# Optimization experiments

Measured on AMD Instinct MI355X. Metric: run time of the kernel, lower is better.

The kernel has to match this reference:

```python
import math
import jax, jax.numpy as jnp
import numpy as np
from jax import lax

N = 224
EPS_BN = 1e-5


def _conv(x, w, b):
    y = lax.conv_general_dilated(x, w, (1, 1), 'SAME',
                                 dimension_numbers=('NCHW', 'OIHW', 'NCHW'))
    return y + b[None, :, None, None]


def _bn(x, g, beta, m, v):
    # eval-mode BatchNorm2d with running stats
    inv = lax.rsqrt(v + EPS_BN)
    return (x - m[None, :, None, None]) * (g * inv)[None, :, None, None] + beta[None, :, None, None]


def _maxpool2(x):
    return lax.reduce_window(x, -jnp.inf, lax.max, (1, 1, 2, 2), (1, 1, 2, 2), 'VALID')


def setup_inputs() -> dict:
    key = jax.random.key(0)
    ks = jax.random.split(key, 12)
    idx = np.arange(N, dtype=np.float32)
    angles = 2.0 * math.pi * idx[None, :] * idx[:, None] / N
    inp = {
        'sequences': jax.random.normal(ks[0], (16, 8, 3, N, N), dtype=jnp.float32),
        'dft_cos': jnp.asarray(np.cos(angles), dtype=jnp.float32),
        'dft_sin': jnp.asarray(np.sin(angles), dtype=jnp.float32),
        'conv1_w': jax.random.normal(ks[1], (16, 3, 3, 3), dtype=jnp.float32) * 0.1,
        'conv1_b': jnp.zeros((16,), jnp.float32),
        'bn1_g': jnp.ones((16,), jnp.float32),
        'bn1_b': jnp.zeros((16,), jnp.float32),
        'bn1_m': jnp.zeros((16,), jnp.float32),
        'bn1_v': jnp.ones((16,), jnp.float32),
        'conv2_w': jax.random.normal(ks[2], (32, 16, 3, 3), dtype=jnp.float32) * 0.05,
        'conv2_b': jnp.zeros((32,), jnp.float32),
        'bn2_g': jnp.ones((32,), jnp.float32),
        'bn2_b': jnp.zeros((32,), jnp.float32),
        'bn2_m': jnp.zeros((32,), jnp.float32),
        'bn2_v': jnp.ones((32,), jnp.float32),
        'conv3_w': jax.random.normal(ks[3], (64, 32, 3, 3), dtype=jnp.float32) * 0.05,
        'conv3_b': jnp.zeros((64,), jnp.float32),
        'bn3_g': jnp.ones((64,), jnp.float32),
        'bn3_b': jnp.zeros((64,), jnp.float32),
        'bn3_m': jnp.zeros((64,), jnp.float32),
        'bn3_v': jnp.ones((64,), jnp.float32),
        'fc_w': jax.random.normal(ks[4], (128, 64), dtype=jnp.float32) * 0.1,
        'fc_b': jnp.zeros((128,), jnp.float32),
    }
    return inp


def reference(sequences, dft_cos, dft_sin,
              conv1_w, conv1_b, bn1_g, bn1_b, bn1_m, bn1_v,
              conv2_w, conv2_b, bn2_g, bn2_b, bn2_m, bn2_v,
              conv3_w, conv3_b, bn3_g, bn3_b, bn3_m, bn3_v,
              fc_w, fc_b):
    b, s = sequences.shape[0], sequences.shape[1]
    x = sequences[:, s // 2]  # center frames [B,3,H,W]

    # 2D DFT via dense matmul chain: X = (C - jS) x (C - jS)
    C, S = dft_cos, dft_sin
    Cx = jnp.einsum('ij,bcjk->bcik', C, x)
    Sx = jnp.einsum('ij,bcjk->bcik', S, x)
    X_real = jnp.einsum('bcij,jk->bcik', Cx, C) - jnp.einsum('bcij,jk->bcik', Sx, S)
    X_imag = -(jnp.einsum('bcij,jk->bcik', Cx, S) + jnp.einsum('bcij,jk->bcik', Sx, C))
    magnitude = jnp.sqrt(X_real ** 2 + X_imag ** 2 + 1e-08)
    spec = jnp.log(magnitude + 1e-08)
    half = N // 2
    spec = jnp.roll(spec, shift=(half, half), axis=(-2, -1))  # fftshift

    # CNN stack (eval-mode BN, dropout disabled)
    h = jax.nn.relu(_bn(_conv(spec, conv1_w, conv1_b), bn1_g, bn1_b, bn1_m, bn1_v))
    h = _maxpool2(h)
    h = jax.nn.relu(_bn(_conv(h, conv2_w, conv2_b), bn2_g, bn2_b, bn2_m, bn2_v))
    h = _maxpool2(h)
    h = jax.nn.relu(_bn(_conv(h, conv3_w, conv3_b), bn3_g, bn3_b, bn3_m, bn3_v))
    h = jnp.mean(h, axis=(2, 3))  # AdaptiveAvgPool2d((1,1)) + flatten -> [B,64]

    freq_out = jax.nn.relu(h @ fc_w.T + fc_b)  # dropout = identity in eval
    return freq_out
```

## Files before the change

kernel.cpp:

```cpp
#include <hip/hip_runtime.h>
#include <math.h>
#include <stddef.h>

#define N224 224
#define PIX 50176
#define ROWS113 25312

__global__ __launch_bounds__(64) void dft1(
    const float* __restrict__ seq, const float* __restrict__ Cm,
    const float* __restrict__ Sm, float* __restrict__ Cx, float* __restrict__ Sx)
{
  const int p = blockIdx.z;
  const int b = p / 3, ch = p % 3;
  const float* __restrict__ x = seq + ((((size_t)b * 8 + 4) * 3 + ch) * PIX);
  const int i0 = blockIdx.y * 32;
  const int k0 = blockIdx.x * 32;
  const int tid = threadIdx.x;
  const int tx = tid & 7, ty = tid >> 3;
  __shared__ float Ctt[16][36], Stt[16][36], Xt[16][36];
  float aC[4][4], aS[4][4];
#pragma unroll
  for (int a = 0; a < 4; ++a)
#pragma unroll
    for (int d = 0; d < 4; ++d) { aC[a][d] = 0.f; aS[a][d] = 0.f; }

  const int sr = tid >> 1;
  const int sk = (tid & 1) * 8;
  const int xj = tid >> 2;
  const int xk = (tid & 3) * 8;

  const float* xbase = x  + (size_t)xj * N224 + k0 + xk;
  const float* cbase = Cm + (size_t)(i0 + sr) * N224 + sk;
  const float* sbase = Sm + (size_t)(i0 + sr) * N224 + sk;

  float4 rx0 = *(const float4*)(xbase);
  float4 rx1 = *(const float4*)(xbase + 4);
  float4 rc0 = *(const float4*)(cbase);
  float4 rc1 = *(const float4*)(cbase + 4);
  float4 rs0 = *(const float4*)(sbase);
  float4 rs1 = *(const float4*)(sbase + 4);

  for (int jt = 0; jt < 14; ++jt) {
    __syncthreads();
    *(float4*)&Xt[xj][xk]     = rx0;
    *(float4*)&Xt[xj][xk + 4] = rx1;
    Ctt[sk+0][sr]=rc0.x; Ctt[sk+1][sr]=rc0.y; Ctt[sk+2][sr]=rc0.z; Ctt[sk+3][sr]=rc0.w;
    Ctt[sk+4][sr]=rc1.x; Ctt[sk+5][sr]=rc1.y; Ctt[sk+6][sr]=rc1.z; Ctt[sk+7][sr]=rc1.w;
    Stt[sk+0][sr]=rs0.x; Stt[sk+1][sr]=rs0.y; Stt[sk+2][sr]=rs0.z; Stt[sk+3][sr]=rs0.w;
    Stt[sk+4][sr]=rs1.x; Stt[sk+5][sr]=rs1.y; Stt[sk+6][sr]=rs1.z; Stt[sk+7][sr]=rs1.w;
    __syncthreads();
    if (jt < 13) {
      const int j = (jt + 1) * 16;
      rx0 = *(const float4*)(xbase + (size_t)j * N224);
      rx1 = *(const float4*)(xbase + (size_t)j * N224 + 4);
      rc0 = *(const float4*)(cbase + j);
      rc1 = *(const float4*)(cbase + j + 4);
      rs0 = *(const float4*)(sbase + j);
      rs1 = *(const float4*)(sbase + j + 4);
    }
#pragma unroll
    for (int jj = 0; jj < 16; ++jj) {
      const float4 cv4 = *(const float4*)&Ctt[jj][4*ty];
      const float4 sv4 = *(const float4*)&Stt[jj][4*ty];
      const float4 xv4 = *(const float4*)&Xt[jj][4*tx];
      const float cva[4] = {cv4.x, cv4.y, cv4.z, cv4.w};
      const float sva[4] = {sv4.x, sv4.y, sv4.z, sv4.w};
      const float xva[4] = {xv4.x, xv4.y, xv4.z, xv4.w};
#pragma unroll
      for (int a = 0; a < 4; ++a)
#pragma unroll
        for (int d = 0; d < 4; ++d) {
          aC[a][d] = fmaf(cva[a], xva[d], aC[a][d]);
          aS[a][d] = fmaf(sva[a], xva[d], aS[a][d]);
        }
    }
  }
  const size_t b113 = (size_t)p * ROWS113;
#pragma unroll
  for (int a = 0; a < 4; ++a) {
    const int i = i0 + 4*ty + a;
    if (i <= 112) {
      const size_t off = b113 + (size_t)i * N224 + k0 + 4*tx;
      *(float4*)&Cx[off] = make_float4(aC[a][0], aC[a][1], aC[a][2], aC[a][3]);
      *(float4*)&Sx[off] = make_float4(aS[a][0], aS[a][1], aS[a][2], aS[a][3]);
    }
  }
}

__global__ __launch_bounds__(64) void dft2(
    const float* __restrict__ Cx, const float* __restrict__ Sx,
    const float* __restrict__ Cm, const float* __restrict__ Sm,
    float* __restrict__ spec)
{
  const int p = blockIdx.z;
  const int i0 = blockIdx.y * 32;
  const int k0 = blockIdx.x * 32;
  const int tid = threadIdx.x;
  const int tx = tid & 7, ty = tid >> 3;
  const size_t b113 = (size_t)p * ROWS113;
  __shared__ float CxT[16][36], SxT[16][36], Ct[16][36], St[16][36];
  float p1[4][4], p2[4][4], p3[4][4], p4[4][4];
#pragma unroll
  for (int a = 0; a < 4; ++a)
#pragma unroll
    for (int d = 0; d < 4; ++d) { p1[a][d]=0.f; p2[a][d]=0.f; p3[a][d]=0.f; p4[a][d]=0.f; }

  const int sr = tid >> 1;
  const int sk = (tid & 1) * 8;
  const int ri = (i0 + sr > 112) ? 112 : i0 + sr;
  const int xj = tid >> 2;
  const int xk = (tid & 3) * 8;

  const float* cxb = Cx + b113 + (size_t)ri * N224 + sk;
  const float* sxb = Sx + b113 + (size_t)ri * N224 + sk;
  const float* ccb = Cm + (size_t)xj * N224 + k0 + xk;
  const float* ssb = Sm + (size_t)xj * N224 + k0 + xk;

  float4 ra0 = *(const float4*)(cxb);
  float4 ra1 = *(const float4*)(cxb + 4);
  float4 rb0 = *(const float4*)(sxb);
  float4 rb1 = *(const float4*)(sxb + 4);
  float4 rc0 = *(const float4*)(ccb);
  float4 rc1 = *(const float4*)(ccb + 4);
  float4 rd0 = *(const float4*)(ssb);
  float4 rd1 = *(const float4*)(ssb + 4);

  for (int jt = 0; jt < 14; ++jt) {
    __syncthreads();
    *(float4*)&Ct[xj][xk]     = rc0;  *(float4*)&Ct[xj][xk + 4] = rc1;
    *(float4*)&St[xj][xk]     = rd0;  *(float4*)&St[xj][xk + 4] = rd1;
    CxT[sk+0][sr]=ra0.x; CxT[sk+1][sr]=ra0.y; CxT[sk+2][sr]=ra0.z; CxT[sk+3][sr]=ra0.w;
    CxT[sk+4][sr]=ra1.x; CxT[sk+5][sr]=ra1.y; CxT[sk+6][sr]=ra1.z; CxT[sk+7][sr]=ra1.w;
    SxT[sk+0][sr]=rb0.x; SxT[sk+1][sr]=rb0.y; SxT[sk+2][sr]=rb0.z; SxT[sk+3][sr]=rb0.w;
    SxT[sk+4][sr]=rb1.x; SxT[sk+5][sr]=rb1.y; SxT[sk+6][sr]=rb1.z; SxT[sk+7][sr]=rb1.w;
    __syncthreads();
    if (jt < 13) {
      const int j = (jt + 1) * 16;
      ra0 = *(const float4*)(cxb + j);
      ra1 = *(const float4*)(cxb + j + 4);
      rb0 = *(const float4*)(sxb + j);
      rb1 = *(const float4*)(sxb + j + 4);
      rc0 = *(const float4*)(ccb + (size_t)j * N224);
      rc1 = *(const float4*)(ccb + (size_t)j * N224 + 4);
      rd0 = *(const float4*)(ssb + (size_t)j * N224);
      rd1 = *(const float4*)(ssb + (size_t)j * N224 + 4);
    }
#pragma unroll
    for (int jj = 0; jj < 16; ++jj) {
      const float4 cx4 = *(const float4*)&CxT[jj][4*ty];
      const float4 sx4 = *(const float4*)&SxT[jj][4*ty];
      const float4 cc4 = *(const float4*)&Ct[jj][4*tx];
      const float4 ss4 = *(const float4*)&St[jj][4*tx];
      const float cxa[4] = {cx4.x, cx4.y, cx4.z, cx4.w};
      const float sxa[4] = {sx4.x, sx4.y, sx4.z, sx4.w};
      const float cca[4] = {cc4.x, cc4.y, cc4.z, cc4.w};
      const float ssa[4] = {ss4.x, ss4.y, ss4.z, ss4.w};
#pragma unroll
      for (int a = 0; a < 4; ++a)
#pragma unroll
        for (int d = 0; d < 4; ++d) {
          p1[a][d] = fmaf(cxa[a], cca[d], p1[a][d]);
          p2[a][d] = fmaf(sxa[a], ssa[d], p2[a][d]);
          p3[a][d] = fmaf(cxa[a], ssa[d], p3[a][d]);
          p4[a][d] = fmaf(sxa[a], cca[d], p4[a][d]);
        }
    }
  }
  const size_t sb = (size_t)p * PIX;
  const int kk0 = k0 + 4*tx;
  const int ok0 = (kk0 < 112) ? kk0 + 112 : kk0 - 112;
#pragma unroll
  for (int a = 0; a < 4; ++a) {
    const int i = i0 + 4*ty + a;
    if (i > 112) continue;
    float sp1[4], sp2[4];
#pragma unroll
    for (int d = 0; d < 4; ++d) {
      const float re = p1[a][d] - p2[a][d];
      const float im = p3[a][d] + p4[a][d];
      sp1[d] = logf(sqrtf(fmaf(re, re, fmaf(im, im, 1e-8f))) + 1e-8f);
      const float re2 = p1[a][d] + p2[a][d];
      const float im2 = p3[a][d] - p4[a][d];
      sp2[d] = logf(sqrtf(fmaf(re2, re2, fmaf(im2, im2, 1e-8f))) + 1e-8f);
    }
    const int oi = (i < 112) ? i + 112 : i - 112;
    *(float4*)&spec[sb + (size_t)oi * N224 + ok0] =
        make_float4(sp1[0], sp1[1], sp1[2], sp1[3]);
    if (i >= 1 && i <= 111)
      *(float4*)&spec[sb + (size_t)(112 - i) * N224 + ok0] =
          make_float4(sp2[0], sp2[1], sp2[2], sp2[3]);
  }
}

__global__ __launch_bounds__(256) void conv1_band(
    const float* __restrict__ spec, const float* __restrict__ w,
    const float* __restrict__ cb, const float* __restrict__ g,
    const float* __restrict__ be, const float* __restrict__ mm,
    const float* __restrict__ vv, float* __restrict__ out)
{
  const int band = blockIdx.x;
  const int b    = blockIdx.y;
  const int tid  = threadIdx.x;
  const int co   = tid & 15;
  const int q    = tid >> 4;
  const int cy0  = band * 2;
  __shared__ float in_t[3][4][228];
  __shared__ float wt[3][9][16];
  for (int i = tid; i < 3*4*224; i += 256) {
    const int x = i % 224, r = (i / 224) % 4, cc = i / 896;
    const int y = cy0 - 1 + r;
    float v = 0.f;
    if (y >= 0 && y < 224)
      v = spec[((size_t)b*3 + cc) * PIX + (size_t)y * N224 + x];
    in_t[cc][r][x+1] = v;
  }
  if (tid < 12) { const int cc = tid / 4, r = tid % 4;
                  in_t[cc][r][0] = 0.f; in_t[cc][r][225] = 0.f; }
  for (int i = tid; i < 3*9*16; i += 256) {
    const int coi = i & 15, k = (i >> 4) % 9, cc = i / 144;
    wt[cc][k][coi] = w[coi*27 + cc*9 + k];
  }
  __syncthreads();
  float acc[2][14];
#pragma unroll
  for (int i = 0; i < 2; ++i)
#pragma unroll
    for (int jx = 0; jx < 14; ++jx) acc[i][jx] = 0.f;
  const int x0 = q * 14;
#pragma unroll
  for (int cc = 0; cc < 3; ++cc) {
    float wr[9];
#pragma unroll
    for (int k = 0; k < 9; ++k) wr[k] = wt[cc][k][co];
#pragma unroll
    for (int rr = 0; rr < 4; ++rr) {
      float xr[16];
      const float2* rp = (const float2*)(&in_t[cc][rr][x0]);
#pragma unroll
      for (int t = 0; t < 8; ++t) { const float2 v = rp[t]; xr[2*t] = v.x; xr[2*t+1] = v.y; }
#pragma unroll
      for (int crow = 0; crow < 2; ++crow) {
        const int krow = rr - crow;
        if (krow < 0 || krow > 2) continue;
#pragma unroll
        for (int xx = 0; xx < 14; ++xx) {
          acc[crow][xx] = fmaf(xr[xx  ], wr[krow*3  ], acc[crow][xx]);
          acc[crow][xx] = fmaf(xr[xx+1], wr[krow*3+1], acc[crow][xx]);
          acc[crow][xx] = fmaf(xr[xx+2], wr[krow*3+2], acc[crow][xx]);
        }
      }
    }
  }
  const float s  = g[co] * rsqrtf(vv[co] + 1e-5f);
  const float sh = be[co] - mm[co]*s;
  const float bb = cb[co];
  const int px0 = q * 7;
#pragma unroll
  for (int px = 0; px < 7; ++px) {
    const float v0 = (acc[0][2*px  ] + bb)*s + sh;
    const float v1 = (acc[0][2*px+1] + bb)*s + sh;
    const float v2 = (acc[1][2*px  ] + bb)*s + sh;
    const float v3 = (acc[1][2*px+1] + bb)*s + sh;
    out[(((size_t)b*16 + co)*112 + band)*112 + px0+px] =
        fmaxf(fmaxf(fmaxf(v0, v1), fmaxf(v2, v3)), 0.f);
  }
}

__global__ __launch_bounds__(256) void conv2_band(
    const float* __restrict__ h1, const float* __restrict__ w,
    const float* __restrict__ cb, const float* __restrict__ g,
    const float* __restrict__ be, const float* __restrict__ mm,
    const float* __restrict__ vv, float* __restrict__ out)
{
  const int band = blockIdx.x;
  const int b    = blockIdx.y;
  const int tid  = threadIdx.x;
  const int co   = tid & 31;
  const int q    = tid >> 5;
  const int cy0  = band * 2;
  __shared__ float in_t[8][4][114];
  __shared__ float wt[8][9][32];
  float acc[2][14];
#pragma unroll
  for (int i = 0; i < 2; ++i)
#pragma unroll
    for (int jx = 0; jx < 14; ++jx) acc[i][jx] = 0.f;

  for (int chunk = 0; chunk < 2; ++chunk) {
    const int ci0 = chunk * 8;
    __syncthreads();
    for (int i = tid; i < 8*4*112; i += 256) {
      const int x = i % 112, r = (i / 112) % 4, cc = i / 448;
      const int y = cy0 - 1 + r;
      float v = 0.f;
      if (y >= 0 && y < 112)
        v = h1[(((size_t)b*16 + ci0+cc)*112 + y)*112 + x];
      in_t[cc][r][x+1] = v;
    }
    if (tid < 32) { const int cc = tid >> 2, r = tid & 3;
                    in_t[cc][r][0] = 0.f; in_t[cc][r][113] = 0.f; }
    for (int i = tid; i < 8*9*32; i += 256) {
      const int coi = i & 31, k = (i >> 5) % 9, cc = i / 288;
      wt[cc][k][coi] = w[coi*144 + (ci0+cc)*9 + k];
    }
    __syncthreads();
    const int x0 = q * 14;
    for (int cc = 0; cc < 8; ++cc) {
      float wr[9];
#pragma unroll
      for (int k = 0; k < 9; ++k) wr[k] = wt[cc][k][co];
#pragma unroll
      for (int rr = 0; rr < 4; ++rr) {
        float xr[16];
        const float2* rp = (const float2*)(&in_t[cc][rr][x0]);
#pragma unroll
        for (int t = 0; t < 8; ++t) { const float2 v = rp[t]; xr[2*t] = v.x; xr[2*t+1] = v.y; }
#pragma unroll
        for (int crow = 0; crow < 2; ++crow) {
          const int krow = rr - crow;
          if (krow < 0 || krow > 2) continue;
#pragma unroll
          for (int x = 0; x < 14; ++x) {
            acc[crow][x] = fmaf(xr[x  ], wr[krow*3  ], acc[crow][x]);
            acc[crow][x] = fmaf(xr[x+1], wr[krow*3+1], acc[crow][x]);
            acc[crow][x] = fmaf(xr[x+2], wr[krow*3+2], acc[crow][x]);
          }
        }
      }
    }
  }
  const float s  = g[co] * rsqrtf(vv[co] + 1e-5f);
  const float sh = be[co] - mm[co]*s;
  const float bb = cb[co];
  const int px0 = q * 7;
#pragma unroll
  for (int px = 0; px < 7; ++px) {
    const float v0 = (acc[0][2*px  ] + bb)*s + sh;
    const float v1 = (acc[0][2*px+1] + bb)*s + sh;
    const float v2 = (acc[1][2*px  ] + bb)*s + sh;
    const float v3 = (acc[1][2*px+1] + bb)*s + sh;
    out[(((size_t)b*32 + co)*56 + band)*56 + px0+px] =
        fmaxf(fmaxf(fmaxf(v0, v1), fmaxf(v2, v3)), 0.f);
  }
}

__global__ __launch_bounds__(256) void conv3_band(
    const float* __restrict__ h2, const float* __restrict__ w,
    const float* __restrict__ cb, const float* __restrict__ g,
    const float* __restrict__ be, const float* __restrict__ mm,
    const float* __restrict__ vv, float* __restrict__ part)
{
  const int band = blockIdx.x;
  const int b    = blockIdx.y;
  const int tid  = threadIdx.x;
  const int co   = tid & 63;
  const int q    = tid >> 6;
  const int y0   = band;
  __shared__ float in_t[8][3][58];
  __shared__ float wt[8][9][64];
  __shared__ float red[4][64];
  float acc[14];
#pragma unroll
  for (int jx = 0; jx < 14; ++jx) acc[jx] = 0.f;

  for (int chunk = 0; chunk < 4; ++chunk) {
    const int ci0 = chunk * 8;
    __syncthreads();
    for (int i = tid; i < 8*3*56; i += 256) {
      const int x = i % 56, r = (i / 56) % 3, cc = i / 168;
      const int y = y0 - 1 + r;
      float v = 0.f;
      if (y >= 0 && y < 56)
        v = h2[(((size_t)b*32 + ci0+cc)*56 + y)*56 + x];
      in_t[cc][r][x+1] = v;
    }
    if (tid < 24) { const int cc = tid / 3, r = tid % 3;
                    in_t[cc][r][0] = 0.f; in_t[cc][r][57] = 0.f; }
    for (int i = tid; i < 8*9*64; i += 256) {
      const int coi = i & 63, k = (i >> 6) % 9, cc = i / 576;
      wt[cc][k][coi] = w[coi*288 + (ci0+cc)*9 + k];
    }
    __syncthreads();
    const int x0 = q * 14;
    for (int cc = 0; cc < 8; ++cc) {
      float wr[9];
#pragma unroll
      for (int k = 0; k < 9; ++k) wr[k] = wt[cc][k][co];
#pragma unroll
      for (int rr = 0; rr < 3; ++rr) {
        float xr[16];
        const float2* rp = (const float2*)(&in_t[cc][rr][x0]);
#pragma unroll
        for (int t = 0; t < 8; ++t) { const float2 v = rp[t]; xr[2*t] = v.x; xr[2*t+1] = v.y; }
#pragma unroll
        for (int x = 0; x < 14; ++x) {
          acc[x] = fmaf(xr[x  ], wr[rr*3  ], acc[x]);
          acc[x] = fmaf(xr[x+1], wr[rr*3+1], acc[x]);
          acc[x] = fmaf(xr[x+2], wr[rr*3+2], acc[x]);
        }
      }
    }
  }
  const float s  = g[co] * rsqrtf(vv[co] + 1e-5f);
  const float sh = be[co] - mm[co]*s;
  const float bb = cb[co];
  float sum = 0.f;
#pragma unroll
  for (int x = 0; x < 14; ++x)
    sum += fmaxf((acc[x] + bb)*s + sh, 0.f);
  red[q][co] = sum;
  __syncthreads();
  if (tid < 64)
    part[(((size_t)b*64 + co)*56) + band] =
        red[0][co] + red[1][co] + red[2][co] + red[3][co];
}

__global__ __launch_bounds__(128) void mean_fc(
    const float* __restrict__ part, const float* __restrict__ fw,
    const float* __restrict__ fb, float* __restrict__ out)
{
  const int b = blockIdx.x;
  const int tid = threadIdx.x;
  __shared__ float h3s[64];
  if (tid < 64) {
    float s = 0.f;
    const float* pp = part + ((size_t)b*64 + tid)*56;
#pragma unroll
    for (int i = 0; i < 56; ++i) s += pp[i];
    h3s[tid] = s * (1.0f / 3136.0f);
  }
  __syncthreads();
  float acc = fb[tid];
#pragma unroll
  for (int c = 0; c < 64; ++c)
    acc = fmaf(h3s[c], fw[tid*64 + c], acc);
  out[b*128 + tid] = fmaxf(acc, 0.f);
}

extern "C" void kernel_launch(void* const* d_in, const int* in_sizes, int n_in,
                              void* d_out, int out_size, void* d_ws, size_t ws_size,
                              hipStream_t stream) {
  const float* seq  = (const float*)d_in[0];
  const float* dcos = (const float*)d_in[1];
  const float* dsin = (const float*)d_in[2];
  const float* c1w  = (const float*)d_in[3];
  const float* c1b  = (const float*)d_in[4];
  const float* b1g  = (const float*)d_in[5];
  const float* b1b  = (const float*)d_in[6];
  const float* b1m  = (const float*)d_in[7];
  const float* b1v  = (const float*)d_in[8];
  const float* c2w  = (const float*)d_in[9];
  const float* c2b  = (const float*)d_in[10];
  const float* b2g  = (const float*)d_in[11];
  const float* b2b  = (const float*)d_in[12];
  const float* b2m  = (const float*)d_in[13];
  const float* b2v  = (const float*)d_in[14];
  const float* c3w  = (const float*)d_in[15];
  const float* c3b  = (const float*)d_in[16];
  const float* b3g  = (const float*)d_in[17];
  const float* b3b  = (const float*)d_in[18];
  const float* b3m  = (const float*)d_in[19];
  const float* b3v  = (const float*)d_in[20];
  const float* fw   = (const float*)d_in[21];
  const float* fb   = (const float*)d_in[22];
  float* out = (float*)d_out;

  float* ws   = (float*)d_ws;
  float* Cx   = ws;
  float* Sx   = ws + 1214976;
  float* spec = ws + 4816896;
  float* h1   = ws;
  float* h2   = ws + 4816896;
  float* part = ws;

  dft1<<<dim3(7, 4, 48), 64, 0, stream>>>(seq, dcos, dsin, Cx, Sx);
  dft2<<<dim3(7, 4, 48), 64, 0, stream>>>(Cx, Sx, dcos, dsin, spec);
  conv1_band<<<dim3(112, 16), 256, 0, stream>>>(spec, c1w, c1b, b1g, b1b, b1m, b1v, h1);
  conv2_band<<<dim3(56, 16), 256, 0, stream>>>(h1, c2w, c2b, b2g, b2b, b2m, b2v, h2);
  conv3_band<<<dim3(56, 16), 256, 0, stream>>>(h2, c3w, c3b, b3g, b3b, b3m, b3v, part);
  mean_fc<<<16, 128, 0, stream>>>(part, fw, fb, out);
}
```

Before: 197.7 us.

## Retile conv kernels with larger per-thread strips and pretransposed weights

Adds a prep kernel that transposes conv weights and folds bias and BatchNorm into scale/shift vectors once per call. Each conv kernel now handles two output bands per block with 28-pixel per-thread strips and float4 shared loads, and reads weights straight from global memory instead of staging them in LDS. Blocks load all input channels at once, so the chunked sync loop goes away. The aim is less LDS traffic and fewer blocks and syncs per output, at the cost of more registers per thread, which may lower occupancy, plus one extra launch.

```diff
diff --git a/kernel.cpp b/kernel.cpp
--- a/kernel.cpp
+++ b/kernel.cpp
@@ -5,6 +5,57 @@
 #define N224 224
 #define PIX 50176
 #define ROWS113 25312
+
+#define OFF_SX    1214976
+#define OFF_SPEC  4816896
+#define OFF_WT    3211264
+#define OFF_WT2   (OFF_WT + 18432)
+#define OFF_WT1   (OFF_WT + 23040)
+#define OFF_SU3   (OFF_WT + 23472)
+#define OFF_SU2   (OFF_WT + 23600)
+#define OFF_SU1   (OFF_WT + 23664)
+#define OFF_PART  (OFF_WT + 32768)
+
+__global__ __launch_bounds__(256) void prep(
+    const float* __restrict__ c1w, const float* __restrict__ c2w,
+    const float* __restrict__ c3w, const float* __restrict__ c1b,
+    const float* __restrict__ c2b, const float* __restrict__ c3b,
+    const float* __restrict__ g1, const float* __restrict__ be1,
+    const float* __restrict__ m1, const float* __restrict__ v1,
+    const float* __restrict__ g2, const float* __restrict__ be2,
+    const float* __restrict__ m2, const float* __restrict__ v2,
+    const float* __restrict__ g3, const float* __restrict__ be3,
+    const float* __restrict__ m3, const float* __restrict__ v3,
+    float* __restrict__ wt3, float* __restrict__ wt2, float* __restrict__ wt1,
+    float* __restrict__ su3, float* __restrict__ su2, float* __restrict__ su1)
+{
+  const int idx = blockIdx.x * 256 + threadIdx.x;
+  const int stride = gridDim.x * 256;
+  for (int i = idx; i < 18432; i += stride) {
+    const int co = i & 63, k = (i >> 6) % 9, cc = i / 576;
+    wt3[i] = c3w[co*288 + cc*9 + k];
+  }
+  for (int i = idx; i < 4608; i += stride) {
+    const int co = i & 31, k = (i >> 5) % 9, cc = i / 288;
+    wt2[i] = c2w[co*144 + cc*9 + k];
+  }
+  for (int i = idx; i < 432; i += stride) {
+    const int co = i & 15, k = (i >> 4) % 9, cc = i / 144;
+    wt1[i] = c1w[co*27 + cc*9 + k];
+  }
+  if (idx < 64) {
+    const float s = g3[idx] * rsqrtf(v3[idx] + 1e-5f);
+    su3[idx] = s; su3[64+idx] = (c3b[idx] - m3[idx]) * s + be3[idx];
+  } else if (idx < 96) {
+    const int c = idx - 64;
+    const float s = g2[c] * rsqrtf(v2[c] + 1e-5f);
+    su2[c] = s; su2[32+c] = (c2b[c] - m2[c]) * s + be2[c];
+  } else if (idx < 112) {
+    const int c = idx - 96;
+    const float s = g1[c] * rsqrtf(v1[c] + 1e-5f);
+    su1[c] = s; su1[16+c] = (c1b[c] - m1[c]) * s + be1[c];
+  }
+}
 
 __global__ __launch_bounds__(64) void dft1(
     const float* __restrict__ seq, const float* __restrict__ Cm,
@@ -192,227 +243,182 @@
   }
 }
 
-__global__ __launch_bounds__(256) void conv1_band(
-    const float* __restrict__ spec, const float* __restrict__ w,
-    const float* __restrict__ cb, const float* __restrict__ g,
-    const float* __restrict__ be, const float* __restrict__ mm,
-    const float* __restrict__ vv, float* __restrict__ out)
-{
-  const int band = blockIdx.x;
-  const int b    = blockIdx.y;
-  const int tid  = threadIdx.x;
-  const int co   = tid & 15;
-  const int q    = tid >> 4;
-  const int cy0  = band * 2;
-  __shared__ float in_t[3][4][228];
-  __shared__ float wt[3][9][16];
-  for (int i = tid; i < 3*4*224; i += 256) {
-    const int x = i % 224, r = (i / 224) % 4, cc = i / 896;
-    const int y = cy0 - 1 + r;
+__global__ __launch_bounds__(256) void conv1(
+    const float* __restrict__ spec, const float* __restrict__ wt1,
+    const float* __restrict__ su1, float* __restrict__ out)
+{
+  const int band = blockIdx.x, b = blockIdx.y;
+  const int tid = threadIdx.x;
+  const int w = tid >> 6, lane = tid & 63;
+  const int co = lane & 15, xsub = lane >> 4;
+  __shared__ float in_t[3][6][232];
+  for (int i = tid; i < 3*6*232; i += 256) {
+    const int c = i % 232, j = (i / 232) % 6, cc = i / 1392;
+    const int y = band*4 - 1 + j, gx = c - 1;
     float v = 0.f;
-    if (y >= 0 && y < 224)
-      v = spec[((size_t)b*3 + cc) * PIX + (size_t)y * N224 + x];
-    in_t[cc][r][x+1] = v;
-  }
-  if (tid < 12) { const int cc = tid / 4, r = tid % 4;
-                  in_t[cc][r][0] = 0.f; in_t[cc][r][225] = 0.f; }
-  for (int i = tid; i < 3*9*16; i += 256) {
-    const int coi = i & 15, k = (i >> 4) % 9, cc = i / 144;
-    wt[cc][k][coi] = w[coi*27 + cc*9 + k];
+    if (c < 226 && y >= 0 && y < 224 && gx >= 0 && gx < 224)
+      v = spec[((size_t)b*3 + cc) * PIX + (size_t)y * N224 + gx];
+    in_t[cc][j][c] = v;
   }
   __syncthreads();
-  float acc[2][14];
-#pragma unroll
-  for (int i = 0; i < 2; ++i)
-#pragma unroll
-    for (int jx = 0; jx < 14; ++jx) acc[i][jx] = 0.f;
-  const int x0 = q * 14;
+  const int pr = w >> 1, xh = w & 1;
+  const int X0 = xh*112 + xsub*28;
+  const int jb = 2*pr;
+  float acc[2][28];
+#pragma unroll
+  for (int r = 0; r < 2; ++r)
+#pragma unroll
+    for (int px = 0; px < 28; ++px) acc[r][px] = 0.f;
 #pragma unroll
   for (int cc = 0; cc < 3; ++cc) {
     float wr[9];
 #pragma unroll
-    for (int k = 0; k < 9; ++k) wr[k] = wt[cc][k][co];
+    for (int k = 0; k < 9; ++k) wr[k] = wt1[(cc*9 + k)*16 + co];
 #pragma unroll
     for (int rr = 0; rr < 4; ++rr) {
-      float xr[16];
-      const float2* rp = (const float2*)(&in_t[cc][rr][x0]);
-#pragma unroll
-      for (int t = 0; t < 8; ++t) { const float2 v = rp[t]; xr[2*t] = v.x; xr[2*t+1] = v.y; }
-#pragma unroll
-      for (int crow = 0; crow < 2; ++crow) {
-        const int krow = rr - crow;
-        if (krow < 0 || krow > 2) continue;
-#pragma unroll
-        for (int xx = 0; xx < 14; ++xx) {
-          acc[crow][xx] = fmaf(xr[xx  ], wr[krow*3  ], acc[crow][xx]);
-          acc[crow][xx] = fmaf(xr[xx+1], wr[krow*3+1], acc[crow][xx]);
-          acc[crow][xx] = fmaf(xr[xx+2], wr[krow*3+2], acc[crow][xx]);
+      float xr[32];
+      const float4* rp = (const float4*)&in_t[cc][jb+rr][X0];
+#pragma unroll
+      for (int t = 0; t < 8; ++t) {
+        const float4 v = rp[t];
+        xr[4*t]=v.x; xr[4*t+1]=v.y; xr[4*t+2]=v.z; xr[4*t+3]=v.w;
+      }
+#pragma unroll
+      for (int cr = 0; cr < 2; ++cr) {
+        const int ky = rr - cr;
+        if (ky < 0 || ky > 2) continue;
+#pragma unroll
+        for (int px = 0; px < 28; ++px) {
+          acc[cr][px] = fmaf(xr[px  ], wr[ky*3  ], acc[cr][px]);
+          acc[cr][px] = fmaf(xr[px+1], wr[ky*3+1], acc[cr][px]);
+          acc[cr][px] = fmaf(xr[px+2], wr[ky*3+2], acc[cr][px]);
         }
       }
     }
   }
-  const float s  = g[co] * rsqrtf(vv[co] + 1e-5f);
-  const float sh = be[co] - mm[co]*s;
-  const float bb = cb[co];
-  const int px0 = q * 7;
-#pragma unroll
-  for (int px = 0; px < 7; ++px) {
-    const float v0 = (acc[0][2*px  ] + bb)*s + sh;
-    const float v1 = (acc[0][2*px+1] + bb)*s + sh;
-    const float v2 = (acc[1][2*px  ] + bb)*s + sh;
-    const float v3 = (acc[1][2*px+1] + bb)*s + sh;
-    out[(((size_t)b*16 + co)*112 + band)*112 + px0+px] =
+  const float s = su1[co], u = su1[16+co];
+  const int py = band*2 + pr, pxb = X0 >> 1;
+#pragma unroll
+  for (int p = 0; p < 14; ++p) {
+    const float v0 = acc[0][2*p]*s + u,   v1 = acc[0][2*p+1]*s + u;
+    const float v2 = acc[1][2*p]*s + u,   v3 = acc[1][2*p+1]*s + u;
+    out[(((size_t)b*16 + co)*112 + py)*112 + pxb + p] =
         fmaxf(fmaxf(fmaxf(v0, v1), fmaxf(v2, v3)), 0.f);
   }
 }
 
-__global__ __launch_bounds__(256) void conv2_band(
-    const float* __restrict__ h1, const float* __restrict__ w,
-    const float* __restrict__ cb, const float* __restrict__ g,
-    const float* __restrict__ be, const float* __restrict__ mm,
-    const float* __restrict__ vv, float* __restrict__ out)
-{
-  const int band = blockIdx.x;
-  const int b    = blockIdx.y;
-  const int tid  = threadIdx.x;
-  const int co   = tid & 31;
-  const int q    = tid >> 5;
-  const int cy0  = band * 2;
-  __shared__ float in_t[8][4][114];
-  __shared__ float wt[8][9][32];
-  float acc[2][14];
-#pragma unroll
-  for (int i = 0; i < 2; ++i)
-#pragma unroll
-    for (int jx = 0; jx < 14; ++jx) acc[i][jx] = 0.f;
-
-  for (int chunk = 0; chunk < 2; ++chunk) {
-    const int ci0 = chunk * 8;
-    __syncthreads();
-    for (int i = tid; i < 8*4*112; i += 256) {
-      const int x = i % 112, r = (i / 112) % 4, cc = i / 448;
-      const int y = cy0 - 1 + r;
-      float v = 0.f;
-      if (y >= 0 && y < 112)
-        v = h1[(((size_t)b*16 + ci0+cc)*112 + y)*112 + x];
-      in_t[cc][r][x+1] = v;
-    }
-    if (tid < 32) { const int cc = tid >> 2, r = tid & 3;
-                    in_t[cc][r][0] = 0.f; in_t[cc][r][113] = 0.f; }
-    for (int i = tid; i < 8*9*32; i += 256) {
-      const int coi = i & 31, k = (i >> 5) % 9, cc = i / 288;
-      wt[cc][k][coi] = w[coi*144 + (ci0+cc)*9 + k];
-    }
-    __syncthreads();
-    const int x0 = q * 14;
-    for (int cc = 0; cc < 8; ++cc) {
-      float wr[9];
-#pragma unroll
-      for (int k = 0; k < 9; ++k) wr[k] = wt[cc][k][co];
-#pragma unroll
-      for (int rr = 0; rr < 4; ++rr) {
-        float xr[16];
-        const float2* rp = (const float2*)(&in_t[cc][rr][x0]);
-#pragma unroll
-        for (int t = 0; t < 8; ++t) { const float2 v = rp[t]; xr[2*t] = v.x; xr[2*t+1] = v.y; }
-#pragma unroll
-        for (int crow = 0; crow < 2; ++crow) {
-          const int krow = rr - crow;
-          if (krow < 0 || krow > 2) continue;
-#pragma unroll
-          for (int x = 0; x < 14; ++x) {
-            acc[crow][x] = fmaf(xr[x  ], wr[krow*3  ], acc[crow][x]);
-            acc[crow][x] = fmaf(xr[x+1], wr[krow*3+1], acc[crow][x]);
-            acc[crow][x] = fmaf(xr[x+2], wr[krow*3+2], acc[crow][x]);
-          }
+__global__ __launch_bounds__(256) void conv2(
+    const float* __restrict__ h1, const float* __restrict__ wt2,
+    const float* __restrict__ su2, float* __restrict__ out)
+{
+  const int band = blockIdx.x, b = blockIdx.y;
+  const int tid = threadIdx.x;
+  const int w = tid >> 6, lane = tid & 63;
+  const int co = lane & 31, xsub = lane >> 5;
+  __shared__ float in_t[16][6][120];
+  for (int i = tid; i < 16*6*120; i += 256) {
+    const int c = i % 120, j = (i / 120) % 6, cc = i / 720;
+    const int y = band*4 - 1 + j, gx = c - 1;
+    float v = 0.f;
+    if (c < 114 && y >= 0 && y < 112 && gx >= 0 && gx < 112)
+      v = h1[(((size_t)b*16 + cc)*112 + y)*112 + gx];
+    in_t[cc][j][c] = v;
+  }
+  __syncthreads();
+  const int pr = w >> 1, xh = w & 1;
+  const int X0 = xh*56 + xsub*28;
+  const int jb = 2*pr;
+  float acc[2][28];
+#pragma unroll
+  for (int r = 0; r < 2; ++r)
+#pragma unroll
+    for (int px = 0; px < 28; ++px) acc[r][px] = 0.f;
+  for (int cc = 0; cc < 16; ++cc) {
+    float wr[9];
+#pragma unroll
+    for (int k = 0; k < 9; ++k) wr[k] = wt2[(cc*9 + k)*32 + co];
+#pragma unroll
+    for (int rr = 0; rr < 4; ++rr) {
+      float xr[32];
+      const float4* rp = (const float4*)&in_t[cc][jb+rr][X0];
+#pragma unroll
+      for (int t = 0; t < 8; ++t) {
+        const float4 v = rp[t];
+        xr[4*t]=v.x; xr[4*t+1]=v.y; xr[4*t+2]=v.z; xr[4*t+3]=v.w;
+      }
+#pragma unroll
+      for (int cr = 0; cr < 2; ++cr) {
+        const int ky = rr - cr;
+        if (ky < 0 || ky > 2) continue;
+#pragma unroll
+        for (int px = 0; px < 28; ++px) {
+          acc[cr][px] = fmaf(xr[px  ], wr[ky*3  ], acc[cr][px]);
+          acc[cr][px] = fmaf(xr[px+1], wr[ky*3+1], acc[cr][px]);
+          acc[cr][px] = fmaf(xr[px+2], wr[ky*3+2], acc[cr][px]);
         }
       }
     }
   }
-  const float s  = g[co] * rsqrtf(vv[co] + 1e-5f);
-  const float sh = be[co] - mm[co]*s;
-  const float bb = cb[co];
-  const int px0 = q * 7;
-#pragma unroll
-  for (int px = 0; px < 7; ++px) {
-    const float v0 = (acc[0][2*px  ] + bb)*s + sh;
-    const float v1 = (acc[0][2*px+1] + bb)*s + sh;
-    const float v2 = (acc[1][2*px  ] + bb)*s + sh;
-    const float v3 = (acc[1][2*px+1] + bb)*s + sh;
-    out[(((size_t)b*32 + co)*56 + band)*56 + px0+px] =
+  const float s = su2[co], u = su2[32+co];
+  const int py = band*2 + pr, pxb = X0 >> 1;
+#pragma unroll
+  for (int p = 0; p < 14; ++p) {
+    const float v0 = acc[0][2*p]*s + u,   v1 = acc[0][2*p+1]*s + u;
+    const float v2 = acc[1][2*p]*s + u,   v3 = acc[1][2*p+1]*s + u;
+    out[(((size_t)b*32 + co)*56 + py)*56 + pxb + p] =
         fmaxf(fmaxf(fmaxf(v0, v1), fmaxf(v2, v3)), 0.f);
   }
 }
 
-__global__ __launch_bounds__(256) void conv3_band(
-    const float* __restrict__ h2, const float* __restrict__ w,
-    const float* __restrict__ cb, const float* __restrict__ g,
-    const float* __restrict__ be, const float* __restrict__ mm,
-    const float* __restrict__ vv, float* __restrict__ part)
-{
-  const int band = blockIdx.x;
-  const int b    = blockIdx.y;
-  const int tid  = threadIdx.x;
-  const int co   = tid & 63;
-  const int q    = tid >> 6;
-  const int y0   = band;
-  __shared__ float in_t[8][3][58];
-  __shared__ float wt[8][9][64];
-  __shared__ float red[4][64];
-  float acc[14];
-#pragma unroll
-  for (int jx = 0; jx < 14; ++jx) acc[jx] = 0.f;
-
-  for (int chunk = 0; chunk < 4; ++chunk) {
-    const int ci0 = chunk * 8;
-    __syncthreads();
-    for (int i = tid; i < 8*3*56; i += 256) {
-      const int x = i % 56, r = (i / 56) % 3, cc = i / 168;
-      const int y = y0 - 1 + r;
-      float v = 0.f;
-      if (y >= 0 && y < 56)
-        v = h2[(((size_t)b*32 + ci0+cc)*56 + y)*56 + x];
-      in_t[cc][r][x+1] = v;
-    }
-    if (tid < 24) { const int cc = tid / 3, r = tid % 3;
-                    in_t[cc][r][0] = 0.f; in_t[cc][r][57] = 0.f; }
-    for (int i = tid; i < 8*9*64; i += 256) {
-      const int coi = i & 63, k = (i >> 6) % 9, cc = i / 576;
-      wt[cc][k][coi] = w[coi*288 + (ci0+cc)*9 + k];
-    }
-    __syncthreads();
-    const int x0 = q * 14;
-    for (int cc = 0; cc < 8; ++cc) {
-      float wr[9];
-#pragma unroll
-      for (int k = 0; k < 9; ++k) wr[k] = wt[cc][k][co];
-#pragma unroll
-      for (int rr = 0; rr < 3; ++rr) {
-        float xr[16];
-        const float2* rp = (const float2*)(&in_t[cc][rr][x0]);
-#pragma unroll
-        for (int t = 0; t < 8; ++t) { const float2 v = rp[t]; xr[2*t] = v.x; xr[2*t+1] = v.y; }
-#pragma unroll
-        for (int x = 0; x < 14; ++x) {
-          acc[x] = fmaf(xr[x  ], wr[rr*3  ], acc[x]);
-          acc[x] = fmaf(xr[x+1], wr[rr*3+1], acc[x]);
-          acc[x] = fmaf(xr[x+2], wr[rr*3+2], acc[x]);
-        }
-      }
-    }
-  }
-  const float s  = g[co] * rsqrtf(vv[co] + 1e-5f);
-  const float sh = be[co] - mm[co]*s;
-  const float bb = cb[co];
+__global__ __launch_bounds__(256) void conv3(
+    const float* __restrict__ h2, const float* __restrict__ wt3,
+    const float* __restrict__ su3, float* __restrict__ part)
+{
+  const int band = blockIdx.x, b = blockIdx.y;
+  const int tid = threadIdx.x;
+  const int w = tid >> 6, co = tid & 63;
+  __shared__ float in_t[32][4][60];
+  for (int i = tid; i < 32*4*60; i += 256) {
+    const int c = i % 60, j = (i / 60) % 4, cc = i / 240;
+    const int y = band*2 - 1 + j, gx = c - 1;
+    float v = 0.f;
+    if (c < 58 && y >= 0 && y < 56 && gx >= 0 && gx < 56)
+      v = h2[(((size_t)b*32 + cc)*56 + y)*56 + gx];
+    in_t[cc][j][c] = v;
+  }
+  __syncthreads();
+  const int rb = w >> 1, xh = w & 1;
+  const int X0 = xh * 28;
+  float acc[28];
+#pragma unroll
+  for (int px = 0; px < 28; ++px) acc[px] = 0.f;
+  for (int cc = 0; cc < 32; ++cc) {
+    float wr[9];
+#pragma unroll
+    for (int k = 0; k < 9; ++k) wr[k] = wt3[(cc*9 + k)*64 + co];
+#pragma unroll
+    for (int rr = 0; rr < 3; ++rr) {
+      float xr[32];
+      const float4* rp = (const float4*)&in_t[cc][rb+rr][X0];
+#pragma unroll
+      for (int t = 0; t < 8; ++t) {
+        const float4 v = rp[t];
+        xr[4*t]=v.x; xr[4*t+1]=v.y; xr[4*t+2]=v.z; xr[4*t+3]=v.w;
+      }
+#pragma unroll
+      for (int px = 0; px < 28; ++px) {
+        acc[px] = fmaf(xr[px  ], wr[rr*3  ], acc[px]);
+        acc[px] = fmaf(xr[px+1], wr[rr*3+1], acc[px]);
+        acc[px] = fmaf(xr[px+2], wr[rr*3+2], acc[px]);
+      }
+    }
+  }
+  const float s = su3[co], u = su3[64+co];
   float sum = 0.f;
 #pragma unroll
-  for (int x = 0; x < 14; ++x)
-    sum += fmaxf((acc[x] + bb)*s + sh, 0.f);
-  red[q][co] = sum;
-  __syncthreads();
-  if (tid < 64)
-    part[(((size_t)b*64 + co)*56) + band] =
-        red[0][co] + red[1][co] + red[2][co] + red[3][co];
+  for (int px = 0; px < 28; ++px)
+    sum += fmaxf(acc[px]*s + u, 0.f);
+  part[((size_t)b*64 + co)*112 + band*4 + w] = sum;
 }
 
 __global__ __launch_bounds__(128) void mean_fc(
@@ -424,9 +430,9 @@
   __shared__ float h3s[64];
   if (tid < 64) {
     float s = 0.f;
-    const float* pp = part + ((size_t)b*64 + tid)*56;
-#pragma unroll
-    for (int i = 0; i < 56; ++i) s += pp[i];
+    const float* pp = part + ((size_t)b*64 + tid)*112;
+#pragma unroll
+    for (int i = 0; i < 112; ++i) s += pp[i];
     h3s[tid] = s * (1.0f / 3136.0f);
   }
   __syncthreads();
@@ -467,16 +473,25 @@
 
   float* ws   = (float*)d_ws;
   float* Cx   = ws;
-  float* Sx   = ws + 1214976;
-  float* spec = ws + 4816896;
+  float* Sx   = ws + OFF_SX;
+  float* spec = ws + OFF_SPEC;
   float* h1   = ws;
-  float* h2   = ws + 4816896;
-  float* part = ws;
-
+  float* h2   = ws + OFF_SPEC;
+  float* wt3  = ws + OFF_WT;
+  float* wt2  = ws + OFF_WT2;
+  float* wt1  = ws + OFF_WT1;
+  float* su3  = ws + OFF_SU3;
+  float* su2  = ws + OFF_SU2;
+  float* su1  = ws + OFF_SU1;
+  float* part = ws + OFF_PART;
+
+  prep<<<24, 256, 0, stream>>>(c1w, c2w, c3w, c1b, c2b, c3b,
+                               b1g, b1b, b1m, b1v, b2g, b2b, b2m, b2v,
+                               b3g, b3b, b3m, b3v, wt3, wt2, wt1, su3, su2, su1);
   dft1<<<dim3(7, 4, 48), 64, 0, stream>>>(seq, dcos, dsin, Cx, Sx);
   dft2<<<dim3(7, 4, 48), 64, 0, stream>>>(Cx, Sx, dcos, dsin, spec);
-  conv1_band<<<dim3(112, 16), 256, 0, stream>>>(spec, c1w, c1b, b1g, b1b, b1m, b1v, h1);
-  conv2_band<<<dim3(56, 16), 256, 0, stream>>>(h1, c2w, c2b, b2g, b2b, b2m, b2v, h2);
-  conv3_band<<<dim3(56, 16), 256, 0, stream>>>(h2, c3w, c3b, b3g, b3b, b3m, b3v, part);
+  conv1<<<dim3(56, 16), 256, 0, stream>>>(spec, wt1, su1, h1);
+  conv2<<<dim3(28, 16), 256, 0, stream>>>(h1, wt2, su2, h2);
+  conv3<<<dim3(28, 16), 256, 0, stream>>>(h2, wt3, su3, part);
   mean_fc<<<16, 128, 0, stream>>>(part, fw, fb, out);
 }
```

New measurement: 198.1 us. Within noise of the previous version (+0.2%).
